# Kernel tuning notes

Hardware: AMD Instinct MI355X
Metric: run time of the kernel (lower is better)

## Reference

```python
import jax, jax.numpy as jnp
import numpy as np

SEQ, D, H, DFF, L, MAXINT = 8, 2, 2, 32, 2, 255
V = MAXINT + 1
BATCH = 131072


def _layer_norm(x, g, b, eps=1e-5):
    mu = jnp.mean(x, axis=-1, keepdims=True)
    var = jnp.mean((x - mu) ** 2, axis=-1, keepdims=True)
    return (x - mu) / jnp.sqrt(var + eps) * g + b


def setup_inputs() -> dict:
    key = jax.random.key(0)
    ks = jax.random.split(key, 8)
    f = lambda k, shape: (jax.random.normal(k, shape, dtype=jnp.float32) * 0.2)
    x = jax.random.randint(ks[0], (BATCH, SEQ), 0, 256)
    return {
        "x": x,
        "Wqkv": f(ks[1], (L, 3 * D, D)), "bqkv": jnp.zeros((L, 3 * D), jnp.float32),
        "Wo": f(ks[2], (L, D, D)), "bo": jnp.zeros((L, D), jnp.float32),
        "W1": f(ks[3], (L, DFF, D)), "b1": jnp.zeros((L, DFF), jnp.float32),
        "W2": f(ks[4], (L, D, DFF)), "b2": jnp.zeros((L, D), jnp.float32),
        "g1": jnp.ones((L, D), jnp.float32), "be1": jnp.zeros((L, D), jnp.float32),
        "g2": jnp.ones((L, D), jnp.float32), "be2": jnp.zeros((L, D), jnp.float32),
        "Wout": f(ks[5], (V, D)), "bout": jnp.zeros((V,), jnp.float32),
    }


def reference(x, Wqkv, bqkv, Wo, bo, W1, b1, W2, b2, g1, be1, g2, be2, Wout, bout):
    B, S = x.shape
    hd = D // H                      # head_dim = 1
    scale = 1.0 / np.sqrt(hd)
    numbers = x.astype(jnp.float32) / MAXINT
    positions = jnp.broadcast_to(jnp.arange(S, dtype=jnp.float32) / (S - 1), (B, S))
    h = jnp.stack([numbers, positions], axis=-1)  # [B, S, D]

    for l in range(L):  # small fixed layer count
        qkv = h @ Wqkv[l].T + bqkv[l]             # [B, S, 3D]
        q, k, v = jnp.split(qkv, 3, axis=-1)
        sh = lambda t: t.reshape(B, S, H, hd).transpose(0, 2, 1, 3)  # [B,H,S,hd]
        q, k, v = sh(q), sh(k), sh(v)
        scores = jnp.einsum('bhqd,bhkd->bhqk', q, k) * scale
        attn = jax.nn.softmax(scores, axis=-1)
        o = jnp.einsum('bhqk,bhkd->bhqd', attn, v)
        o = o.transpose(0, 2, 1, 3).reshape(B, S, D) @ Wo[l].T + bo[l]
        h = _layer_norm(h + o, g1[l], be1[l])      # post-norm (norm_first=False)
        ff = jax.nn.gelu(h @ W1[l].T + b1[l], approximate=False) @ W2[l].T + b2[l]
        h = _layer_norm(h + ff, g2[l], be2[l])

    final = h[:, -1]                               # [B, D]
    return final @ Wout.T + bout                   # [B, V]
```

## Files before the change

### kernel.cpp

```cpp
#include <hip/hip_runtime.h>
#include <math.h>

#define SEQ   8
#define DFF   32
#define NL    2
#define VOCAB 256
#define BATCH 131072
#define TBL_N 4096

__device__ __forceinline__ void ff_eval(
    const float* __restrict__ W1, const float* __restrict__ b1,
    const float* __restrict__ W2, const float* __restrict__ b2,
    const float* __restrict__ g1, const float* __restrict__ be1,
    int l, float nd, float& f0, float& f1)
{
    float h0 = fmaf( nd, g1[l*2+0], be1[l*2+0]);
    float h1 = fmaf(-nd, g1[l*2+1], be1[l*2+1]);
    f0 = b2[l*2+0];
    f1 = b2[l*2+1];
    const float* w1p = W1 + l*64;
    const float* b1p = b1 + l*32;
    const float* w2p = W2 + l*64;
    for (int j = 0; j < DFF; ++j) {
        float t = fmaf(w1p[j*2], h0, fmaf(w1p[j*2+1], h1, b1p[j]));
        float g = 0.5f * t * (1.0f + erff(t * 0.70710678118654752f));
        f0 = fmaf(g, w2p[j], f0);
        f1 = fmaf(g, w2p[32+j], f1);
    }
}

__global__ __launch_bounds__(256) void build_tables(
    const float* __restrict__ W1, const float* __restrict__ b1,
    const float* __restrict__ W2, const float* __restrict__ b2,
    const float* __restrict__ g1, const float* __restrict__ be1,
    float4* __restrict__ T4)
{
    int idx = blockIdx.x * 256 + threadIdx.x;
    if (idx >= NL * TBL_N) return;
    int l = idx >> 12;
    int i = idx & (TBL_N - 1);
    float nd0 = -1.0f + (float)i       * (2.0f / TBL_N);
    float nd1 = -1.0f + (float)(i + 1) * (2.0f / TBL_N);
    float a0, a1, c0, c1;
    ff_eval(W1, b1, W2, b2, g1, be1, l, nd0, a0, a1);
    ff_eval(W1, b1, W2, b2, g1, be1, l, nd1, c0, c1);
    T4[idx] = make_float4(a0, a1, c0, c1);
}

__global__ __launch_bounds__(256, 4) void seqtx_main(
    const int*   __restrict__ x,
    const float* __restrict__ Wqkv, const float* __restrict__ bqkv,
    const float* __restrict__ Wo,   const float* __restrict__ bo,
    const float* __restrict__ g1,   const float* __restrict__ be1,
    const float* __restrict__ g2,   const float* __restrict__ be2,
    const float* __restrict__ Wout, const float* __restrict__ bout,
    const float4* __restrict__ T4,
    float* __restrict__ out)
{
    __shared__ float snd[32];

    const int tid = threadIdx.x;
    const int sub = tid & 7;
    const int gid = blockIdx.x * 256 + tid;

    float h0 = (float)x[gid] * (1.0f / 255.0f);
    float h1 = (float)sub * (1.0f / 7.0f);
    float ndl = 0.0f;

    #pragma unroll
    for (int l = 0; l < NL; ++l) {
        const float* wq = Wqkv + l * 12;
        const float* bq = bqkv + l * 6;
        float q0 = fmaf(wq[0],  h0, fmaf(wq[1],  h1, bq[0]));
        float q1 = fmaf(wq[2],  h0, fmaf(wq[3],  h1, bq[1]));
        float k0 = fmaf(wq[4],  h0, fmaf(wq[5],  h1, bq[2]));
        float k1 = fmaf(wq[6],  h0, fmaf(wq[7],  h1, bq[3]));
        float v0 = fmaf(wq[8],  h0, fmaf(wq[9],  h1, bq[4]));
        float v1 = fmaf(wq[10], h0, fmaf(wq[11], h1, bq[5]));

        float q0e = q0 * 1.44269504f;
        float q1e = q1 * 1.44269504f;
        float s0 = 0.0f, a0 = 0.0f, s1 = 0.0f, a1 = 0.0f;
        #pragma unroll
        for (int j = 0; j < SEQ; ++j) {
            float kj0 = __shfl(k0, j, SEQ);
            float vj0 = __shfl(v0, j, SEQ);
            float e0  = __builtin_amdgcn_exp2f(q0e * kj0);
            s0 += e0;  a0 = fmaf(e0, vj0, a0);
            float kj1 = __shfl(k1, j, SEQ);
            float vj1 = __shfl(v1, j, SEQ);
            float e1  = __builtin_amdgcn_exp2f(q1e * kj1);
            s1 += e1;  a1 = fmaf(e1, vj1, a1);
        }
        float o0 = a0 * __builtin_amdgcn_rcpf(s0);
        float o1 = a1 * __builtin_amdgcn_rcpf(s1);

        const float* wo = Wo + l * 4;
        float p0 = fmaf(wo[0], o0, fmaf(wo[1], o1, bo[l * 2 + 0]));
        float p1 = fmaf(wo[2], o0, fmaf(wo[3], o1, bo[l * 2 + 1]));
        float a = h0 + p0, c = h1 + p1;
        float d = 0.5f * (a - c);
        float nd = d * __builtin_amdgcn_rsqf(fmaf(d, d, 1e-5f));
        h0 = fmaf( nd, g1[l * 2 + 0], be1[l * 2 + 0]);
        h1 = fmaf(-nd, g1[l * 2 + 1], be1[l * 2 + 1]);

        float tf = fmaf(nd, (float)(TBL_N / 2), (float)(TBL_N / 2));
        int   i  = (int)tf;
        i = (i < 0) ? 0 : ((i > TBL_N - 1) ? TBL_N - 1 : i);
        float fr = tf - (float)i;
        float4 e4 = T4[l * TBL_N + i];
        float f0 = fmaf(fr, e4.z - e4.x, e4.x);
        float f1 = fmaf(fr, e4.w - e4.y, e4.y);

        a = h0 + f0;  c = h1 + f1;
        d = 0.5f * (a - c);
        float nd2 = d * __builtin_amdgcn_rsqf(fmaf(d, d, 1e-5f));
        h0 = fmaf( nd2, g2[l * 2 + 0], be2[l * 2 + 0]);
        h1 = fmaf(-nd2, g2[l * 2 + 1], be2[l * 2 + 1]);
        ndl = nd2;
    }

    if (sub == SEQ - 1) snd[tid >> 3] = ndl;
    __syncthreads();

    const int r  = tid >> 6;
    const int cg = (tid & 63) * 4;

    const float2* wvp = reinterpret_cast<const float2*>(Wout);
    float2 wv0 = wvp[cg + 0];
    float2 wv1 = wvp[cg + 1];
    float2 wv2 = wvp[cg + 2];
    float2 wv3 = wvp[cg + 3];
    float4 bv  = *reinterpret_cast<const float4*>(bout + cg);
    float gf0 = g2[2], gf1 = g2[3], bf0 = be2[2], bf1 = be2[3];

    float u0 = wv0.x * gf0 - wv0.y * gf1,  w0 = fmaf(wv0.x, bf0, fmaf(wv0.y, bf1, bv.x));
    float u1 = wv1.x * gf0 - wv1.y * gf1,  w1 = fmaf(wv1.x, bf0, fmaf(wv1.y, bf1, bv.y));
    float u2 = wv2.x * gf0 - wv2.y * gf1,  w2 = fmaf(wv2.x, bf0, fmaf(wv2.y, bf1, bv.z));
    float u3 = wv3.x * gf0 - wv3.y * gf1,  w3 = fmaf(wv3.x, bf0, fmaf(wv3.y, bf1, bv.w));

    const size_t rowbase = (size_t)blockIdx.x * 32;
    #pragma unroll
    for (int it = 0; it < 8; ++it) {
        int row = it * 4 + r;
        float ndv = snd[row];
        float4 res;
        res.x = fmaf(ndv, u0, w0);
        res.y = fmaf(ndv, u1, w1);
        res.z = fmaf(ndv, u2, w2);
        res.w = fmaf(ndv, u3, w3);
        *reinterpret_cast<float4*>(&out[(rowbase + row) * VOCAB + cg]) = res;
    }
}

extern "C" void kernel_launch(void* const* d_in, const int* in_sizes, int n_in,
                              void* d_out, int out_size, void* d_ws, size_t ws_size,
                              hipStream_t stream) {
    const int*   x    = (const int*)  d_in[0];
    const float* Wqkv = (const float*)d_in[1];
    const float* bqkv = (const float*)d_in[2];
    const float* Wo   = (const float*)d_in[3];
    const float* bo   = (const float*)d_in[4];
    const float* W1   = (const float*)d_in[5];
    const float* b1   = (const float*)d_in[6];
    const float* W2   = (const float*)d_in[7];
    const float* b2   = (const float*)d_in[8];
    const float* g1   = (const float*)d_in[9];
    const float* be1  = (const float*)d_in[10];
    const float* g2   = (const float*)d_in[11];
    const float* be2  = (const float*)d_in[12];
    const float* Wout = (const float*)d_in[13];
    const float* bout = (const float*)d_in[14];
    float* out = (float*)d_out;

    float4* T4 = (float4*)d_ws;

    build_tables<<<(NL * TBL_N + 255) / 256, 256, 0, stream>>>(
        W1, b1, W2, b2, g1, be1, T4);

    seqtx_main<<<BATCH / 32, 256, 0, stream>>>(
        x, Wqkv, bqkv, Wo, bo, g1, be1, g2, be2, Wout, bout, T4, out);
}
```

Before: 40.90 us.

## Parallelize FF table build across DFF lanes with shuffle reduction

The lookup-table build kernel now gives each table entry 32 threads, one per hidden unit, and combines the partial sums with warp xor-shuffles, where before one thread looped serially over 32 hidden units. This removes a long serial erf chain from a kernel that only launched 32 blocks, leaving most of the GPU idle. The main kernel's launch bounds also change from 4 to 8 blocks per SM, which may cap registers. The table kernel now does 32x more thread launches and shuffle traffic in exchange for parallelism.

```diff
diff --git a/kernel.cpp b/kernel.cpp
--- a/kernel.cpp
+++ b/kernel.cpp
@@ -8,46 +8,50 @@
 #define BATCH 131072
 #define TBL_N 4096
 
-__device__ __forceinline__ void ff_eval(
+__global__ __launch_bounds__(256) void build_tables_par(
     const float* __restrict__ W1, const float* __restrict__ b1,
     const float* __restrict__ W2, const float* __restrict__ b2,
     const float* __restrict__ g1, const float* __restrict__ be1,
-    int l, float nd, float& f0, float& f1)
+    const float* __restrict__ b2b,
+    float4* __restrict__ T4)
 {
-    float h0 = fmaf( nd, g1[l*2+0], be1[l*2+0]);
-    float h1 = fmaf(-nd, g1[l*2+1], be1[l*2+1]);
-    f0 = b2[l*2+0];
-    f1 = b2[l*2+1];
-    const float* w1p = W1 + l*64;
-    const float* b1p = b1 + l*32;
-    const float* w2p = W2 + l*64;
-    for (int j = 0; j < DFF; ++j) {
-        float t = fmaf(w1p[j*2], h0, fmaf(w1p[j*2+1], h1, b1p[j]));
-        float g = 0.5f * t * (1.0f + erff(t * 0.70710678118654752f));
-        f0 = fmaf(g, w2p[j], f0);
-        f1 = fmaf(g, w2p[32+j], f1);
+    int gt    = blockIdx.x * 256 + threadIdx.x;
+    int entry = gt >> 5;
+    int j     = gt & 31;
+    if (entry >= NL * TBL_N) return;
+    int l = entry >> 12;
+    int i = entry & (TBL_N - 1);
+
+    float nd0 = -1.0f + (float)i * (2.0f / TBL_N);
+    float nd1 = nd0 + (2.0f / TBL_N);
+
+    float ga = g1[l*2+0], gb = g1[l*2+1], ba = be1[l*2+0], bb = be1[l*2+1];
+    float w1a = W1[l*64 + j*2], w1b = W1[l*64 + j*2 + 1], b1j = b1[l*32 + j];
+    float w2a = W2[l*64 + j],   w2b = W2[l*64 + 32 + j];
+
+    float h0 = fmaf( nd0, ga, ba), h1 = fmaf(-nd0, gb, bb);
+    float t  = fmaf(w1a, h0, fmaf(w1b, h1, b1j));
+    float g  = 0.5f * t * (1.0f + erff(t * 0.70710678118654752f));
+    float f00 = g * w2a, f10 = g * w2b;
+    h0 = fmaf( nd1, ga, ba); h1 = fmaf(-nd1, gb, bb);
+    t  = fmaf(w1a, h0, fmaf(w1b, h1, b1j));
+    g  = 0.5f * t * (1.0f + erff(t * 0.70710678118654752f));
+    float f01 = g * w2a, f11 = g * w2b;
+
+    #pragma unroll
+    for (int m = 1; m < 32; m <<= 1) {
+        f00 += __shfl_xor(f00, m, 32);
+        f10 += __shfl_xor(f10, m, 32);
+        f01 += __shfl_xor(f01, m, 32);
+        f11 += __shfl_xor(f11, m, 32);
+    }
+    if (j == 0) {
+        T4[entry] = make_float4(f00 + b2b[l*2+0], f10 + b2b[l*2+1],
+                                f01 + b2b[l*2+0], f11 + b2b[l*2+1]);
     }
 }
 
-__global__ __launch_bounds__(256) void build_tables(
-    const float* __restrict__ W1, const float* __restrict__ b1,
-    const float* __restrict__ W2, const float* __restrict__ b2,
-    const float* __restrict__ g1, const float* __restrict__ be1,
-    float4* __restrict__ T4)
-{
-    int idx = blockIdx.x * 256 + threadIdx.x;
-    if (idx >= NL * TBL_N) return;
-    int l = idx >> 12;
-    int i = idx & (TBL_N - 1);
-    float nd0 = -1.0f + (float)i       * (2.0f / TBL_N);
-    float nd1 = -1.0f + (float)(i + 1) * (2.0f / TBL_N);
-    float a0, a1, c0, c1;
-    ff_eval(W1, b1, W2, b2, g1, be1, l, nd0, a0, a1);
-    ff_eval(W1, b1, W2, b2, g1, be1, l, nd1, c0, c1);
-    T4[idx] = make_float4(a0, a1, c0, c1);
-}
-
-__global__ __launch_bounds__(256, 4) void seqtx_main(
+__global__ __launch_bounds__(256, 8) void seqtx_main(
     const int*   __restrict__ x,
     const float* __restrict__ Wqkv, const float* __restrict__ bqkv,
     const float* __restrict__ Wo,   const float* __restrict__ bo,
@@ -175,8 +179,8 @@
 
     float4* T4 = (float4*)d_ws;
 
-    build_tables<<<(NL * TBL_N + 255) / 256, 256, 0, stream>>>(
-        W1, b1, W2, b2, g1, be1, T4);
+    build_tables_par<<<(NL * TBL_N * 32) / 256, 256, 0, stream>>>(
+        W1, b1, W2, b2, g1, be1, b2, T4);
 
     seqtx_main<<<BATCH / 32, 256, 0, stream>>>(
         x, Wqkv, bqkv, Wo, bo, g1, be1, g2, be2, Wout, bout, T4, out);
```

Result: faster. 33.95 us (-17.0%).
